# Kernel tuning notes

Hardware: AMD Instinct MI355X
Metric: run time of the kernel (lower is better)

Reference implementation:

```python
import jax, jax.numpy as jnp
import numpy as np

B, IN, OUT = 8192, 1024, 1024


def setup_inputs() -> dict:
    key = jax.random.key(0)
    k1, k2 = jax.random.split(key)
    x = jax.random.normal(k1, (B, IN), dtype=jnp.float32)
    W_seed = jax.random.normal(k2, (IN, OUT), dtype=jnp.float32) / np.sqrt(IN).astype(np.float32)
    b_seed = jnp.zeros((OUT,), dtype=jnp.float32)
    W_sig = jnp.zeros((2,), dtype=jnp.float32)  # mixture logits over ['dense','Toeplitz']
    b_sig = jnp.zeros((2,), dtype=jnp.float32)  # mixture logits over ['dense','None']
    A_sig = jnp.zeros((2,), dtype=jnp.float32)  # mixture logits over ['linear','relu']
    return {"x": x, "W_seed": W_seed, "b_seed": b_seed,
            "W_sig": W_sig, "b_sig": b_sig, "A_sig": A_sig}


def _toeplitz_from_seed(W_seed):
    # seed_vec = [W_seed[0, out-1], ..., W_seed[0, 1], W_seed[0,0], ..., W_seed[in-1,0]]
    in_sz, out_sz = W_seed.shape
    seed_vec = jnp.concatenate([W_seed[0, -1:0:-1], W_seed[:, 0]])  # [out-1 + in]
    # W_toep[i, j] = seed_vec[i - j + out - 1]
    idx = jnp.arange(in_sz)[:, None] - jnp.arange(out_sz)[None, :] + (out_sz - 1)
    return seed_vec[idx]  # [in, out]


def reference(x, W_seed, b_seed, W_sig, b_sig, A_sig):
    W_toep = _toeplitz_from_seed(W_seed)
    w_s = jax.nn.softmax(W_sig)
    W_core = w_s[0] * W_seed + w_s[1] * W_toep          # softmax-weighted weight mixture
    b_s = jax.nn.softmax(b_sig)
    b_core = b_s[0] * b_seed                             # 'None' branch contributes zeros
    out = x @ W_core + b_core                            # [B, out]
    a_s = jax.nn.softmax(A_sig)
    return a_s[0] * out + a_s[1] * jax.nn.relu(out)      # activation mixture
```

## Files before the change

### kernel.cpp

```cpp
#include <hip/hip_runtime.h>

typedef unsigned short ushort_t;
typedef __bf16 bf16x8 __attribute__((ext_vector_type(8)));
typedef float f32x4 __attribute__((ext_vector_type(4)));

#define AS1 __attribute__((address_space(1)))
#define AS3 __attribute__((address_space(3)))

__device__ __forceinline__ ushort_t f2bf(float f) {
    unsigned u = __builtin_bit_cast(unsigned, f);
    u = (u + 0x7fffu + ((u >> 16) & 1u)) >> 16;
    return (ushort_t)u;
}

__device__ __forceinline__ void async16(void* lds, const void* g) {
    __builtin_amdgcn_global_load_lds((const AS1 unsigned int*)g,
                                     (AS3 unsigned int*)lds, 16, 0, 0);
}

__device__ __forceinline__ void softmax2(const float* __restrict__ sig, float& s0, float& s1) {
    float a = sig[0], b = sig[1];
    float m = fmaxf(a, b);
    float e0 = __expf(a - m), e1 = __expf(b - m);
    float inv = 1.0f / (e0 + e1);
    s0 = e0 * inv; s1 = e1 * inv;
}

__device__ __forceinline__ float toep_val(const float* __restrict__ Wseed, int k, int o) {
    return (k >= o) ? Wseed[(size_t)(k - o) << 10] : Wseed[o - k];
}

__global__ __launch_bounds__(256) void prep_kernel(const float* __restrict__ x,
                                                   const float* __restrict__ Wseed,
                                                   const float* __restrict__ Wsig,
                                                   ushort_t* __restrict__ xb,
                                                   ushort_t* __restrict__ Wt) {
    int b = blockIdx.x;
    if (b < 4096) {
        int i = b * 256 + threadIdx.x;
        const float4* xp = (const float4*)x + (size_t)i * 2;
        float4 a = xp[0], c = xp[1];
        uint4 r;
        r.x = (unsigned)f2bf(a.x) | ((unsigned)f2bf(a.y) << 16);
        r.y = (unsigned)f2bf(a.z) | ((unsigned)f2bf(a.w) << 16);
        r.z = (unsigned)f2bf(c.x) | ((unsigned)f2bf(c.y) << 16);
        r.w = (unsigned)f2bf(c.z) | ((unsigned)f2bf(c.w) << 16);
        ((uint4*)xb)[i] = r;
        return;
    }
    __shared__ float T[64][65];
    int bb = b - 4096;
    int k0 = (bb >> 4) * 64;
    int o0 = (bb & 15) * 64;
    int t = threadIdx.x;
    #pragma unroll
    for (int i = 0; i < 4; ++i) {
        int lin = t + i * 256;
        int kr = lin >> 4;
        int c4 = lin & 15;
        float4 v = *(const float4*)&Wseed[(size_t)(k0 + kr) * 1024 + o0 + c4 * 4];
        T[kr][c4 * 4 + 0] = v.x;
        T[kr][c4 * 4 + 1] = v.y;
        T[kr][c4 * 4 + 2] = v.z;
        T[kr][c4 * 4 + 3] = v.w;
    }
    __syncthreads();
    float s0, s1; softmax2(Wsig, s0, s1);
    #pragma unroll
    for (int i = 0; i < 2; ++i) {
        int lin = t + i * 256;
        int oo = lin >> 3;
        int kq = (lin & 7) * 8;
        unsigned r[4];
        #pragma unroll
        for (int q = 0; q < 4; ++q) {
            float v0 = s0 * T[kq + 2 * q + 0][oo] + s1 * toep_val(Wseed, k0 + kq + 2 * q + 0, o0 + oo);
            float v1 = s0 * T[kq + 2 * q + 1][oo] + s1 * toep_val(Wseed, k0 + kq + 2 * q + 1, o0 + oo);
            r[q] = (unsigned)f2bf(v0) | ((unsigned)f2bf(v1) << 16);
        }
        *(uint4*)&Wt[(size_t)(o0 + oo) * 1024 + k0 + kq] = make_uint4(r[0], r[1], r[2], r[3]);
    }
}

#define BM 128
#define BN 128
#define BK 32
#define NKT 32

__global__ __launch_bounds__(256, 2) void gemm_kernel(const ushort_t* __restrict__ Xb,
                                                      const ushort_t* __restrict__ Wt,
                                                      const float* __restrict__ bseed,
                                                      const float* __restrict__ bsig,
                                                      const float* __restrict__ asig,
                                                      float* __restrict__ out) {
    __shared__ ushort_t lds[16384];
    ushort_t* At0 = lds;
    ushort_t* Bt0 = lds + 4096;
    ushort_t* At1 = lds + 8192;
    ushort_t* Bt1 = lds + 12288;

    const int t = threadIdx.x;
    const int wv = t >> 6;
    const int lane = t & 63;

    const int orig = blockIdx.x;
    const int g = orig & 7;
    const int within = orig >> 3;
    const int rb = g * 8 + (within >> 3);
    const int cb = within & 7;
    const int brow = rb * BM;
    const int bcol = cb * BN;

    const int r0 = t >> 2;
    const int kc = (t & 3) * 8;
    const ushort_t* gA0 = Xb + (size_t)(brow + r0) * 1024 + kc;
    const ushort_t* gA1 = Xb + (size_t)(brow + 64 + r0) * 1024 + kc;
    const ushort_t* gB0 = Wt + (size_t)(bcol + r0) * 1024 + kc;
    const ushort_t* gB1 = Wt + (size_t)(bcol + 64 + r0) * 1024 + kc;

    f32x4 acc[4][4];
    #pragma unroll
    for (int i = 0; i < 4; ++i)
        #pragma unroll
        for (int j = 0; j < 4; ++j) acc[i][j] = (f32x4){0.f, 0.f, 0.f, 0.f};

    const int wr = (wv >> 1) * 64;
    const int wcn = (wv & 1) * 64;
    const int fr = lane & 15;
    const int kg = (lane >> 4) * 8;

    const int sA = wv * 512;
    const int sA2 = 2048 + wv * 512;
#define STAGE(Abuf, Bbuf, ko)                                  \
    do {                                                       \
        async16((Abuf) + sA,  gA0 + (ko));                     \
        async16((Abuf) + sA2, gA1 + (ko));                     \
        async16((Bbuf) + sA,  gB0 + (ko));                     \
        async16((Bbuf) + sA2, gB1 + (ko));                     \
    } while (0)

#define COMPUTE(Abuf, Bbuf)                                                        \
    do {                                                                           \
        bf16x8 af[4], bf[4];                                                       \
        _Pragma("unroll")                                                          \
        for (int mi = 0; mi < 4; ++mi)                                             \
            af[mi] = *(const bf16x8*)&(Abuf)[(wr + mi * 16 + fr) * BK + kg];       \
        _Pragma("unroll")                                                          \
        for (int ni = 0; ni < 4; ++ni)                                             \
            bf[ni] = *(const bf16x8*)&(Bbuf)[(wcn + ni * 16 + fr) * BK + kg];      \
        _Pragma("unroll")                                                          \
        for (int mi = 0; mi < 4; ++mi)                                             \
            _Pragma("unroll")                                                      \
            for (int ni = 0; ni < 4; ++ni)                                         \
                acc[mi][ni] = __builtin_amdgcn_mfma_f32_16x16x32_bf16(             \
                    af[mi], bf[ni], acc[mi][ni], 0, 0, 0);                         \
    } while (0)

    STAGE(At0, Bt0, 0);
    __syncthreads();
    for (int it = 0; it < 15; ++it) {
        STAGE(At1, Bt1, (2 * it + 1) * BK);
        COMPUTE(At0, Bt0);
        __syncthreads();
        STAGE(At0, Bt0, (2 * it + 2) * BK);
        COMPUTE(At1, Bt1);
        __syncthreads();
    }
    STAGE(At1, Bt1, 31 * BK);
    COMPUTE(At0, Bt0);
    __syncthreads();
    COMPUTE(At1, Bt1);

    float bs0, bs1, as0, as1;
    softmax2(bsig, bs0, bs1);
    softmax2(asig, as0, as1);

    #pragma unroll
    for (int ni = 0; ni < 4; ++ni) {
        int col = bcol + wcn + ni * 16 + fr;
        float bias = bs0 * bseed[col];
        #pragma unroll
        for (int mi = 0; mi < 4; ++mi) {
            int row = brow + wr + mi * 16 + (lane >> 4) * 4;
            #pragma unroll
            for (int r = 0; r < 4; ++r) {
                float v = acc[mi][ni][r] + bias;
                out[(size_t)(row + r) * 1024 + col] = as0 * v + as1 * fmaxf(v, 0.f);
            }
        }
    }
#undef STAGE
#undef COMPUTE
}

__global__ __launch_bounds__(256) void naive_kernel(const float* __restrict__ x,
                                                    const float* __restrict__ Wseed,
                                                    const float* __restrict__ bseed,
                                                    const float* __restrict__ Wsig,
                                                    const float* __restrict__ bsig,
                                                    const float* __restrict__ asig,
                                                    float* __restrict__ out) {
    int idx = blockIdx.x * 256 + threadIdx.x;
    int b = idx >> 10, o = idx & 1023;
    float ws0, ws1, bs0, bs1, as0, as1;
    softmax2(Wsig, ws0, ws1);
    softmax2(bsig, bs0, bs1);
    softmax2(asig, as0, as1);
    float s = 0.f;
    const float* xr = x + (size_t)b * 1024;
    for (int k = 0; k < 1024; ++k) {
        float wc = ws0 * Wseed[((size_t)k << 10) + o] + ws1 * toep_val(Wseed, k, o);
        s += xr[k] * wc;
    }
    float v = s + bs0 * bseed[o];
    out[idx] = as0 * v + as1 * fmaxf(v, 0.f);
}

extern "C" void kernel_launch(void* const* d_in, const int* in_sizes, int n_in,
                              void* d_out, int out_size, void* d_ws, size_t ws_size,
                              hipStream_t stream) {
    const float* x     = (const float*)d_in[0];
    const float* Wseed = (const float*)d_in[1];
    const float* bseed = (const float*)d_in[2];
    const float* Wsig  = (const float*)d_in[3];
    const float* bsig  = (const float*)d_in[4];
    const float* Asig  = (const float*)d_in[5];
    float* out = (float*)d_out;

    const size_t need = (2u << 20) + (16u << 20) + 1024;
    if (ws_size < need) {
        naive_kernel<<<dim3(8192 * 1024 / 256), dim3(256), 0, stream>>>(
            x, Wseed, bseed, Wsig, bsig, Asig, out);
        return;
    }

    ushort_t* Wt = (ushort_t*)d_ws;
    ushort_t* Xb = (ushort_t*)((char*)d_ws + (2u << 20));

    prep_kernel<<<dim3(4096 + 256), dim3(256), 0, stream>>>(x, Wseed, Wsig, Xb, Wt);
    gemm_kernel<<<dim3(512), dim3(256), 0, stream>>>(Xb, Wt, bseed, bsig, Asig, out);
}
```

Before: 42.93 us.

## Fuse fp32-to-bf16 conversion of x into GEMM A-tile staging

Removes the separate pass that converted x to bf16 in workspace; the GEMM now loads fp32 x tiles into registers, converts to bf16, and writes them to LDS, while W stays on async LDS loads. This eliminates a full write and reread of the bf16 activation copy and shrinks the workspace. In exchange the GEMM reads twice as many bytes for A per tile and spends registers and ALU on conversion, with A loads no longer using the direct-to-LDS path.

```diff
diff --git a/kernel.cpp b/kernel.cpp
--- a/kernel.cpp
+++ b/kernel.cpp
@@ -30,26 +30,11 @@
     return (k >= o) ? Wseed[(size_t)(k - o) << 10] : Wseed[o - k];
 }
 
-__global__ __launch_bounds__(256) void prep_kernel(const float* __restrict__ x,
-                                                   const float* __restrict__ Wseed,
-                                                   const float* __restrict__ Wsig,
-                                                   ushort_t* __restrict__ xb,
-                                                   ushort_t* __restrict__ Wt) {
-    int b = blockIdx.x;
-    if (b < 4096) {
-        int i = b * 256 + threadIdx.x;
-        const float4* xp = (const float4*)x + (size_t)i * 2;
-        float4 a = xp[0], c = xp[1];
-        uint4 r;
-        r.x = (unsigned)f2bf(a.x) | ((unsigned)f2bf(a.y) << 16);
-        r.y = (unsigned)f2bf(a.z) | ((unsigned)f2bf(a.w) << 16);
-        r.z = (unsigned)f2bf(c.x) | ((unsigned)f2bf(c.y) << 16);
-        r.w = (unsigned)f2bf(c.z) | ((unsigned)f2bf(c.w) << 16);
-        ((uint4*)xb)[i] = r;
-        return;
-    }
+__global__ __launch_bounds__(256) void prep_w_kernel(const float* __restrict__ Wseed,
+                                                     const float* __restrict__ Wsig,
+                                                     ushort_t* __restrict__ Wt) {
     __shared__ float T[64][65];
-    int bb = b - 4096;
+    int bb = blockIdx.x;
     int k0 = (bb >> 4) * 64;
     int o0 = (bb & 15) * 64;
     int t = threadIdx.x;
@@ -87,7 +72,7 @@
 #define BK 32
 #define NKT 32
 
-__global__ __launch_bounds__(256, 2) void gemm_kernel(const ushort_t* __restrict__ Xb,
+__global__ __launch_bounds__(256, 2) void gemm_kernel(const float* __restrict__ Xf,
                                                       const ushort_t* __restrict__ Wt,
                                                       const float* __restrict__ bseed,
                                                       const float* __restrict__ bsig,
@@ -113,8 +98,8 @@
 
     const int r0 = t >> 2;
     const int kc = (t & 3) * 8;
-    const ushort_t* gA0 = Xb + (size_t)(brow + r0) * 1024 + kc;
-    const ushort_t* gA1 = Xb + (size_t)(brow + 64 + r0) * 1024 + kc;
+    const float* gX0 = Xf + (size_t)(brow + r0) * 1024 + kc;
+    const float* gX1 = Xf + (size_t)(brow + 64 + r0) * 1024 + kc;
     const ushort_t* gB0 = Wt + (size_t)(bcol + r0) * 1024 + kc;
     const ushort_t* gB1 = Wt + (size_t)(bcol + 64 + r0) * 1024 + kc;
 
@@ -131,12 +116,34 @@
 
     const int sA = wv * 512;
     const int sA2 = 2048 + wv * 512;
-#define STAGE(Abuf, Bbuf, ko)                                  \
-    do {                                                       \
-        async16((Abuf) + sA,  gA0 + (ko));                     \
-        async16((Abuf) + sA2, gA1 + (ko));                     \
-        async16((Bbuf) + sA,  gB0 + (ko));                     \
-        async16((Bbuf) + sA2, gB1 + (ko));                     \
+    f32x4 ar0, ar1, ar2, ar3;
+
+#define LOADA(ko)                                          \
+    do {                                                   \
+        ar0 = *(const f32x4*)(gX0 + (ko));                 \
+        ar1 = *(const f32x4*)(gX0 + (ko) + 4);             \
+        ar2 = *(const f32x4*)(gX1 + (ko));                 \
+        ar3 = *(const f32x4*)(gX1 + (ko) + 4);             \
+    } while (0)
+
+#define WRITEA(Abuf)                                       \
+    do {                                                   \
+        bf16x8 v0, v1;                                     \
+        _Pragma("unroll")                                  \
+        for (int j = 0; j < 4; ++j) {                      \
+            v0[j]     = (__bf16)ar0[j];                    \
+            v0[4 + j] = (__bf16)ar1[j];                    \
+            v1[j]     = (__bf16)ar2[j];                    \
+            v1[4 + j] = (__bf16)ar3[j];                    \
+        }                                                  \
+        *(bf16x8*)&(Abuf)[t * 8] = v0;                     \
+        *(bf16x8*)&(Abuf)[2048 + t * 8] = v1;              \
+    } while (0)
+
+#define STAGEB(Bbuf, ko)                                   \
+    do {                                                   \
+        async16((Bbuf) + sA,  gB0 + (ko));                 \
+        async16((Bbuf) + sA2, gB1 + (ko));                 \
     } while (0)
 
 #define COMPUTE(Abuf, Bbuf)                                                        \
@@ -156,18 +163,26 @@
                     af[mi], bf[ni], acc[mi][ni], 0, 0, 0);                         \
     } while (0)
 
-    STAGE(At0, Bt0, 0);
+    LOADA(0);
+    STAGEB(Bt0, 0);
+    WRITEA(At0);
     __syncthreads();
     for (int it = 0; it < 15; ++it) {
-        STAGE(At1, Bt1, (2 * it + 1) * BK);
+        LOADA((2 * it + 1) * BK);
+        STAGEB(Bt1, (2 * it + 1) * BK);
         COMPUTE(At0, Bt0);
+        WRITEA(At1);
         __syncthreads();
-        STAGE(At0, Bt0, (2 * it + 2) * BK);
+        LOADA((2 * it + 2) * BK);
+        STAGEB(Bt0, (2 * it + 2) * BK);
         COMPUTE(At1, Bt1);
+        WRITEA(At0);
         __syncthreads();
     }
-    STAGE(At1, Bt1, 31 * BK);
+    LOADA(31 * BK);
+    STAGEB(Bt1, 31 * BK);
     COMPUTE(At0, Bt0);
+    WRITEA(At1);
     __syncthreads();
     COMPUTE(At1, Bt1);
 
@@ -189,7 +204,9 @@
             }
         }
     }
-#undef STAGE
+#undef LOADA
+#undef WRITEA
+#undef STAGEB
 #undef COMPUTE
 }
 
@@ -227,7 +244,7 @@
     const float* Asig  = (const float*)d_in[5];
     float* out = (float*)d_out;
 
-    const size_t need = (2u << 20) + (16u << 20) + 1024;
+    const size_t need = (2u << 20) + 1024;
     if (ws_size < need) {
         naive_kernel<<<dim3(8192 * 1024 / 256), dim3(256), 0, stream>>>(
             x, Wseed, bseed, Wsig, bsig, Asig, out);
@@ -235,8 +252,7 @@
     }
 
     ushort_t* Wt = (ushort_t*)d_ws;
-    ushort_t* Xb = (ushort_t*)((char*)d_ws + (2u << 20));
-
-    prep_kernel<<<dim3(4096 + 256), dim3(256), 0, stream>>>(x, Wseed, Wsig, Xb, Wt);
-    gemm_kernel<<<dim3(512), dim3(256), 0, stream>>>(Xb, Wt, bseed, bsig, Asig, out);
-}
+
+    prep_w_kernel<<<dim3(256), dim3(256), 0, stream>>>(Wseed, Wsig, Wt);
+    gemm_kernel<<<dim3(512), dim3(256), 0, stream>>>(x, Wt, bseed, bsig, Asig, out);
+}
```

New measurement: 51.61 us. 1.2x slower.
